# Optimization experiments

Measured on AMD Instinct MI355X. Metric: run time of the kernel, lower is better.

Reference implementation:

```python
import jax, jax.numpy as jnp
import numpy as np

C = 4096
C8 = C // 8  # 512, must equal h*w
B, H, W = 32, 16, 32


def setup_inputs() -> dict:
    key = jax.random.key(0)
    ks = jax.random.split(key, 8)
    s = 0.02
    return {
        "x": jax.random.normal(ks[0], (B, C, H, W), dtype=jnp.float32),
        "Wq": jax.random.normal(ks[1], (C8, C), dtype=jnp.float32) * s,
        "bq": jax.random.normal(ks[2], (C8,), dtype=jnp.float32) * s,
        "Wk": jax.random.normal(ks[3], (C8, C), dtype=jnp.float32) * s,
        "bk": jax.random.normal(ks[4], (C8,), dtype=jnp.float32) * s,
        "Wv": jax.random.normal(ks[5], (C, C), dtype=jnp.float32) * s,
        "bv": jax.random.normal(ks[6], (C,), dtype=jnp.float32) * s,
        "gamma": jax.random.normal(ks[7], (1,), dtype=jnp.float32),
    }


def reference(x, Wq, bq, Wk, bk, Wv, bv, gamma):
    b, c, h, w = x.shape
    xf = x.reshape(b, c, h * w)               # (b, c, hw)
    # 1x1 conv == per-position linear over channels
    q = jnp.einsum("oc,bcl->bol", Wq, xf) + bq[None, :, None]   # (b, c8, hw)
    k = jnp.einsum("oc,bcl->bol", Wk, xf) + bk[None, :, None]   # (b, c8, hw)
    v = jnp.einsum("oc,bcl->bol", Wv, xf) + bv[None, :, None]   # (b, c, hw)
    # energy = bmm(Q, K^T): (b, c8, c8); no sqrt(d) scaling (faithful)
    energy = jnp.einsum("bol,bpl->bop", q, k)
    attn = jax.nn.softmax(energy, axis=-1)
    # out = bmm(V, attn^T): out[b,c,p] = sum_k V[b,c,k] * attn[b,p,k]
    out = jnp.einsum("bck,bpk->bcp", v, attn)  # requires hw == c8
    out = out.reshape(b, c, h, w)
    return gamma * out + x
```

## Files before the change

### kernel.cpp

```cpp
#include <hip/hip_runtime.h>


typedef _Float16 f16;
typedef _Float16 h8 __attribute__((ext_vector_type(8)));
typedef _Float16 h4 __attribute__((ext_vector_type(4)));
typedef float fx4 __attribute__((ext_vector_type(4)));

#define CC  4096
#define C8  512
#define HWD 512
#define NB  32


__device__ __forceinline__ h8 ldfragC(const char* s, int row, int cb) {
  const int b = ((row << 7) | cb) ^ ((row & 7) << 4);
  return *reinterpret_cast<const h8*>(s + b);
}

#define AS1C(p) ((const __attribute__((address_space(1))) unsigned int*)(p))
#define AS3(p)  ((__attribute__((address_space(3))) unsigned int*)(p))

#define STAGE(bufsel) { \
  char* la_ = smem + ((bufsel) << 16); \
  char* lb_ = la_ + 32768; \
  _Pragma("unroll") for (int q = 0; q < 4; ++q) { \
    __builtin_amdgcn_global_load_lds(AS1C(pA[q]), AS3(la_ + (q << 13) + w1024), 16, 0, 0); \
    __builtin_amdgcn_global_load_lds(AS1C(pB[q]), AS3(lb_ + (q << 13) + w1024), 16, 0, 0); \
    pA[q] += 128; pB[q] += 128; } }

#define LOADA(hm, kh) { \
  _Pragma("unroll") for (int f = 0; f < 4; ++f) \
    a[f] = ldfragC(At, wr * 128 + (hm) * 64 + f * 16 + frow, (kh) * 64 + kq); }

#define LOADB(kh) { \
  _Pragma("unroll") for (int g = 0; g < 4; ++g) \
    b[g] = ldfragC(Bt, wc * 64 + g * 16 + frow, (kh) * 64 + kq); }

#define PHASE(hm) { \
  asm volatile("s_barrier" ::: "memory"); \
  asm volatile("s_waitcnt lgkmcnt(0)" ::: "memory"); \
  __builtin_amdgcn_sched_barrier(0); \
  __builtin_amdgcn_s_setprio(1); \
  _Pragma("unroll") for (int f = 0; f < 4; ++f) \
  _Pragma("unroll") for (int g = 0; g < 4; ++g) \
    acc[(hm) * 4 + f][g] = __builtin_amdgcn_mfma_f32_16x16x32_f16( \
        a[f], b[g], acc[(hm) * 4 + f][g], 0, 0, 0); \
  __builtin_amdgcn_s_setprio(0); \
  asm volatile("s_barrier" ::: "memory"); }

template<int EPI>
__global__ __launch_bounds__(512, 2) void gemm256(
    const f16* __restrict__ Ah, const f16* __restrict__ Bh,
    int lda, int ldb, long sAb, long sBb, long sCb, int ldc, int K,
    const float* __restrict__ bias, float* __restrict__ Cf, f16* __restrict__ Ch,
    const float* __restrict__ resid, const float* __restrict__ gam)
{
  extern __shared__ __align__(16) char smem[];
  const int F  = blockIdx.x;
  const int Vv = ((F & 7) << 7) | (F >> 3);
  const int bz = Vv >> 5;
  const int m0 = (Vv & 15) << 8;
  const int n0 = ((Vv >> 4) & 1) << 8;

  const int T = threadIdx.x;
  const int lane = T & 63;
  const int w = T >> 6;
  const int wr = w >> 2, wc = w & 3;
  const int frow = lane & 15;
  const int kq = (lane >> 4) << 4;
  const int w1024 = w << 10;

  const int rr = T >> 3;
  const int corig = ((T & 7) << 4) ^ ((rr & 7) << 4);
  const char* pA[4];
  const char* pB[4];
#pragma unroll
  for (int q = 0; q < 4; ++q) {
    pA[q] = (const char*)(Ah + bz * sAb + (long)(m0 + q * 64 + rr) * lda) + corig;
    pB[q] = (const char*)(Bh + bz * sBb + (long)(n0 + q * 64 + rr) * ldb) + corig;
  }

  fx4 acc[8][4] = {};
  const int nt = K >> 6;

  STAGE(0)
  for (int t = 0; t < nt; ++t) {
    const int cur = t & 1;
    if (t + 1 < nt) {
      STAGE(cur ^ 1)
      asm volatile("s_waitcnt vmcnt(8)" ::: "memory");
    } else {
      asm volatile("s_waitcnt vmcnt(0)" ::: "memory");
    }
    asm volatile("s_barrier" ::: "memory");
    const char* At = smem + (cur << 16);
    const char* Bt = At + 32768;
    h8 a[4], b[4];
    LOADA(0, 0) LOADB(0)
    PHASE(0)
    LOADA(1, 0)
    PHASE(1)
    LOADA(0, 1) LOADB(1)
    PHASE(0)
    LOADA(1, 1)
    PHASE(1)
  }

  const int cm = (lane >> 4) << 2;
  const int cn = lane & 15;
  const float g0 = (EPI == 3) ? gam[0] : 0.f;
#pragma unroll
  for (int fm = 0; fm < 8; ++fm) {
    const int gr0 = m0 + wr * 128 + fm * 16 + cm;
#pragma unroll
    for (int fn = 0; fn < 4; ++fn) {
      const int gc = n0 + wc * 64 + fn * 16 + cn;
#pragma unroll
      for (int j = 0; j < 4; ++j) {
        const long ci = bz * sCb + (long)(gr0 + j) * ldc + gc;
        if constexpr (EPI == 1) Ch[ci] = (f16)(acc[fm][fn][j] + bias[gr0 + j]);
        else                    Cf[ci] = g0 * acc[fm][fn][j] + resid[ci];
      }
    }
  }
}

__device__ __forceinline__ void stage_tile(const f16* __restrict__ g, f16* __restrict__ s, int ld) {
  const int t = threadIdx.x;
#pragma unroll
  for (int i = 0; i < 4; ++i) {
    const int id = t + i * 256;
    const int r = id >> 3, j = id & 7;
    const uint4 v = *reinterpret_cast<const uint4*>(g + (long)r * ld + (j << 3));
    char* p = reinterpret_cast<char*>(s);
    const int b = ((r << 7) + (j << 4)) ^ ((r & 7) << 4);
    *reinterpret_cast<uint4*>(p + b) = v;
  }
}

__device__ __forceinline__ h8 ldfrag(const f16* s, int row, int kb) {
  const int b = ((row << 7) + kb) ^ ((row & 7) << 4);
  return *reinterpret_cast<const h8*>(reinterpret_cast<const char*>(s) + b);
}

template<int EPI>
__global__ __launch_bounds__(256) void gemm_tri(
    const f16* __restrict__ Ah, const f16* __restrict__ Al,
    const f16* __restrict__ Bh, const f16* __restrict__ Bl,
    int K, int lda, int ldb, long sAb, long sBb, long sCb, int ldc,
    const float* __restrict__ bias,
    float* __restrict__ Cf, f16* __restrict__ Ch, f16* __restrict__ Cl)
{
  constexpr int TILE = 128 * 64;
  __shared__ __align__(16) f16 smem[4 * TILE];
  f16* sAh = smem;
  f16* sBh = smem + TILE;
  f16* sAl = smem + 2 * TILE;
  f16* sBl = smem + 3 * TILE;

  const int bz = blockIdx.z;
  const int m0 = blockIdx.y * 128, n0 = blockIdx.x * 128;
  const f16* gA = Ah + (long)bz * sAb + (long)m0 * lda;
  const f16* gB = Bh + (long)bz * sBb + (long)n0 * ldb;

  const int lane = threadIdx.x & 63;
  const int wid  = threadIdx.x >> 6;
  const int wr = wid >> 1, wc = wid & 1;
  const int frow = lane & 15;
  const int kq = (lane >> 4) << 4;

  fx4 acc[4][4] = {};

  for (int k0 = 0; k0 < K; k0 += 64) {
    stage_tile(gA + k0, sAh, lda);
    stage_tile(gB + k0, sBh, ldb);
    stage_tile(Al + (long)bz * sAb + (long)m0 * lda + k0, sAl, lda);
    stage_tile(Bl + (long)bz * sBb + (long)n0 * ldb + k0, sBl, ldb);
    __syncthreads();
#pragma unroll
    for (int ks = 0; ks < 2; ++ks) {
      const int kb = ks * 64 + kq;
      h8 aH[4], bH[4], aL[4], bL[4];
#pragma unroll
      for (int f = 0; f < 4; ++f) {
        aH[f] = ldfrag(sAh, wr * 64 + f * 16 + frow, kb);
        bH[f] = ldfrag(sBh, wc * 64 + f * 16 + frow, kb);
        aL[f] = ldfrag(sAl, wr * 64 + f * 16 + frow, kb);
        bL[f] = ldfrag(sBl, wc * 64 + f * 16 + frow, kb);
      }
#pragma unroll
      for (int fm = 0; fm < 4; ++fm)
#pragma unroll
        for (int fn = 0; fn < 4; ++fn) {
          acc[fm][fn] = __builtin_amdgcn_mfma_f32_16x16x32_f16(aH[fm], bH[fn], acc[fm][fn], 0, 0, 0);
          acc[fm][fn] = __builtin_amdgcn_mfma_f32_16x16x32_f16(aH[fm], bL[fn], acc[fm][fn], 0, 0, 0);
          acc[fm][fn] = __builtin_amdgcn_mfma_f32_16x16x32_f16(aL[fm], bH[fn], acc[fm][fn], 0, 0, 0);
        }
    }
    __syncthreads();
  }

  const int cm = (lane >> 4) * 4;
  const int cn = lane & 15;
#pragma unroll
  for (int fm = 0; fm < 4; ++fm) {
    const int gr0 = m0 + wr * 64 + fm * 16 + cm;
#pragma unroll
    for (int fn = 0; fn < 4; ++fn) {
      const int gc = n0 + wc * 64 + fn * 16 + cn;
#pragma unroll
      for (int j = 0; j < 4; ++j) {
        const int gr = gr0 + j;
        const long ci = (long)bz * sCb + (long)gr * ldc + gc;
        float v = acc[fm][fn][j];
        if constexpr (EPI == 0) {
          v += bias[gr];
          const f16 h = (f16)v;
          Ch[ci] = h;
          Cl[ci] = (f16)(v - (float)h);
        } else {
          Cf[ci] = v;
        }
      }
    }
  }
}

__global__ void transpose_split_k(const float* __restrict__ x, f16* __restrict__ xh, f16* __restrict__ xl) {
  __shared__ float t[32][33];
  const int l0 = blockIdx.x * 32, c0 = blockIdx.y * 32;
  const long bi = (long)blockIdx.z * CC * HWD;
  const long bo = (long)blockIdx.z * HWD * CC;
  const int tx = threadIdx.x, ty = threadIdx.y;
#pragma unroll
  for (int i = 0; i < 32; i += 8)
    t[ty + i][tx] = x[bi + (long)(c0 + ty + i) * HWD + l0 + tx];
  __syncthreads();
#pragma unroll
  for (int i = 0; i < 32; i += 8) {
    const float v = t[tx][ty + i];
    const f16 h = (f16)v;
    const long o = bo + (long)(l0 + ty + i) * CC + c0 + tx;
    xh[o] = h;
    xl[o] = (f16)(v - (float)h);
  }
}

template<bool HASLO>
__global__ void split_k(const float* __restrict__ in, f16* __restrict__ hi, f16* __restrict__ lo, long n) {
  const long i = ((long)blockIdx.x * blockDim.x + threadIdx.x) * 4;
  if (i >= n) return;
  const float4 v = *reinterpret_cast<const float4*>(in + i);
  const float vv[4] = {v.x, v.y, v.z, v.w};
  h4 h, l;
#pragma unroll
  for (int j = 0; j < 4; ++j) {
    const f16 hh = (f16)vv[j];
    h[j] = hh;
    l[j] = (f16)(vv[j] - (float)hh);
  }
  *reinterpret_cast<h4*>(hi + i) = h;
  if constexpr (HASLO) *reinterpret_cast<h4*>(lo + i) = l;
}

__global__ __launch_bounds__(256) void softmax_k(const float* __restrict__ E, f16* __restrict__ attn) {
  const int lane = threadIdx.x & 63;
  const int wid  = threadIdx.x >> 6;
  const long row = (long)blockIdx.x * 4 + wid;
  const float* e = E + row * 512;
  const float4 a = *reinterpret_cast<const float4*>(e + lane * 8);
  const float4 b = *reinterpret_cast<const float4*>(e + lane * 8 + 4);
  float vv[8] = {a.x, a.y, a.z, a.w, b.x, b.y, b.z, b.w};
  float m = vv[0];
#pragma unroll
  for (int i = 1; i < 8; ++i) m = fmaxf(m, vv[i]);
#pragma unroll
  for (int s = 32; s > 0; s >>= 1) m = fmaxf(m, __shfl_xor(m, s));
  float sum = 0.f;
  float ex[8];
#pragma unroll
  for (int i = 0; i < 8; ++i) { ex[i] = __expf(vv[i] - m); sum += ex[i]; }
#pragma unroll
  for (int s = 32; s > 0; s >>= 1) sum += __shfl_xor(sum, s);
  const float inv = 1.f / sum;
  h8 o;
#pragma unroll
  for (int i = 0; i < 8; ++i) o[i] = (f16)(ex[i] * inv);
  *reinterpret_cast<h8*>(attn + row * 512 + lane * 8) = o;
}

extern "C" void kernel_launch(void* const* d_in, const int* in_sizes, int n_in,
                              void* d_out, int out_size, void* d_ws, size_t ws_size,
                              hipStream_t stream) {
  const float* x  = (const float*)d_in[0];
  const float* Wq = (const float*)d_in[1];
  const float* bq = (const float*)d_in[2];
  const float* Wk = (const float*)d_in[3];
  const float* bk = (const float*)d_in[4];
  const float* Wv = (const float*)d_in[5];
  const float* bv = (const float*)d_in[6];
  const float* gm = (const float*)d_in[7];
  float* out = (float*)d_out;

  const size_t szXT = (size_t)NB * HWD * CC;
  const size_t szQK = (size_t)NB * C8 * HWD;
  const size_t szW  = (size_t)C8 * CC;
  const size_t szWv = (size_t)CC * CC;
  const size_t needBytes = (2 * szXT + 4 * szQK + 4 * szW + szWv) * sizeof(f16);
  if (ws_size < needBytes) return;

  f16* xT_h = (f16*)d_ws;
  f16* xT_l = xT_h + szXT;
  f16* v16  = xT_l;
  f16* q_h  = xT_h + 2 * szXT;
  f16* q_l  = q_h + szQK;
  f16* k_h  = q_l + szQK;
  f16* k_l  = k_h + szQK;
  f16* wq_h = k_l + szQK;
  f16* wq_l = wq_h + szW;
  f16* wk_h = wq_l + szW;
  f16* wk_l = wk_h + szW;
  f16* attn = wq_h;
  f16* wv_h = wk_l + szW;
  float* E  = (float*)wv_h;

  split_k<true ><<<dim3((C8 * CC) / 1024), 256, 0, stream>>>(Wq, wq_h, wq_l, (long)C8 * CC);
  split_k<true ><<<dim3((C8 * CC) / 1024), 256, 0, stream>>>(Wk, wk_h, wk_l, (long)C8 * CC);
  split_k<false><<<dim3((CC * CC) / 1024), 256, 0, stream>>>(Wv, wv_h, nullptr, (long)CC * CC);
  transpose_split_k<<<dim3(HWD / 32, CC / 32, NB), dim3(32, 8), 0, stream>>>(x, xT_h, xT_l);
  gemm_tri<0><<<dim3(4, 4, NB), 256, 0, stream>>>(wq_h, wq_l, xT_h, xT_l, CC, CC, CC,
      0L, (long)HWD * CC, (long)C8 * HWD, HWD, bq, nullptr, q_h, q_l);
  gemm_tri<0><<<dim3(4, 4, NB), 256, 0, stream>>>(wk_h, wk_l, xT_h, xT_l, CC, CC, CC,
      0L, (long)HWD * CC, (long)C8 * HWD, HWD, bk, nullptr, k_h, k_l);
  gemm256<1><<<dim3(1024), 512, 131072, stream>>>(wv_h, xT_h, CC, CC,
      0L, (long)HWD * CC, (long)CC * HWD, HWD, CC, bv, nullptr, v16, nullptr, nullptr);
  gemm_tri<2><<<dim3(4, 4, NB), 256, 0, stream>>>(q_h, q_l, k_h, k_l, HWD, HWD, HWD,
      (long)C8 * HWD, (long)C8 * HWD, (long)C8 * C8, C8, nullptr, E, nullptr, nullptr);
  softmax_k<<<dim3(NB * C8 / 4), 256, 0, stream>>>(E, attn);
  gemm256<3><<<dim3(1024), 512, 131072, stream>>>(v16, attn, HWD, HWD,
      (long)CC * HWD, (long)C8 * HWD, (long)CC * HWD, HWD, C8, nullptr, out, nullptr, x, gm);
}
```

Baseline: 1.384 ms.

## Interleave next-tile global-to-LDS prefetch across MMA phases in GEMM main loop

Restructures the K loop so the global_load_lds prefetch of the next tile is split into pieces issued between the LDS fragment reads and MFMA phases, rather than all at once at the top of each iteration. Fragment registers are double-buffered (a0/a1, b0/b1), and the loop is unrolled by two with a fixed buffer index per half. The aim is to spread memory traffic across compute and overlap it better. The trade-off is a full vmcnt(0) wait at each tile start and more barriers, which may expose load latency. The unroll assumes an even number of K tiles.

```diff
diff --git a/kernel.cpp b/kernel.cpp
--- a/kernel.cpp
+++ b/kernel.cpp
@@ -20,7 +20,7 @@
 #define AS1C(p) ((const __attribute__((address_space(1))) unsigned int*)(p))
 #define AS3(p)  ((__attribute__((address_space(3))) unsigned int*)(p))
 
-#define STAGE(bufsel) { \
+#define STAGE_ALL(bufsel) { \
   char* la_ = smem + ((bufsel) << 16); \
   char* lb_ = la_ + 32768; \
   _Pragma("unroll") for (int q = 0; q < 4; ++q) { \
@@ -28,25 +28,63 @@
     __builtin_amdgcn_global_load_lds(AS1C(pB[q]), AS3(lb_ + (q << 13) + w1024), 16, 0, 0); \
     pA[q] += 128; pB[q] += 128; } }
 
-#define LOADA(hm, kh) { \
+#define STAGE2(bufsel, q) { \
+  char* la_ = smem + ((bufsel) << 16); \
+  char* lb_ = la_ + 32768; \
+  __builtin_amdgcn_global_load_lds(AS1C(pA[q]), AS3(la_ + ((q) << 13) + w1024), 16, 0, 0); \
+  __builtin_amdgcn_global_load_lds(AS1C(pB[q]), AS3(lb_ + ((q) << 13) + w1024), 16, 0, 0); \
+  pA[q] += 128; pB[q] += 128; }
+
+#define DSREADS_A(dst, hm, kh) \
   _Pragma("unroll") for (int f = 0; f < 4; ++f) \
-    a[f] = ldfragC(At, wr * 128 + (hm) * 64 + f * 16 + frow, (kh) * 64 + kq); }
-
-#define LOADB(kh) { \
+    dst[f] = ldfragC(At, wr * 128 + (hm) * 64 + f * 16 + frow, (kh) * 64 + kq);
+
+#define DSREADS_B(dst, kh) \
   _Pragma("unroll") for (int g = 0; g < 4; ++g) \
-    b[g] = ldfragC(Bt, wc * 64 + g * 16 + frow, (kh) * 64 + kq); }
-
-#define PHASE(hm) { \
-  asm volatile("s_barrier" ::: "memory"); \
-  asm volatile("s_waitcnt lgkmcnt(0)" ::: "memory"); \
-  __builtin_amdgcn_sched_barrier(0); \
+    dst[g] = ldfragC(Bt, wc * 64 + g * 16 + frow, (kh) * 64 + kq);
+
+#define MMA16(hm, av, bv) \
   __builtin_amdgcn_s_setprio(1); \
   _Pragma("unroll") for (int f = 0; f < 4; ++f) \
   _Pragma("unroll") for (int g = 0; g < 4; ++g) \
     acc[(hm) * 4 + f][g] = __builtin_amdgcn_mfma_f32_16x16x32_f16( \
-        a[f], b[g], acc[(hm) * 4 + f][g], 0, 0, 0); \
-  __builtin_amdgcn_s_setprio(0); \
-  asm volatile("s_barrier" ::: "memory"); }
+        av[f], bv[g], acc[(hm) * 4 + f][g], 0, 0, 0); \
+  __builtin_amdgcn_s_setprio(0);
+
+#define KTILE(cur, DOSTAGE) { \
+  const bool dost_ = (DOSTAGE); \
+  const char* At = smem + ((cur) << 16); \
+  const char* Bt = At + 32768; \
+  h8 a0[4], a1[4], b0[4], b1[4]; \
+  asm volatile("s_waitcnt vmcnt(0)" ::: "memory"); \
+  __builtin_amdgcn_s_barrier(); \
+   \
+  DSREADS_A(a0, 0, 0) DSREADS_B(b0, 0) \
+  if (dost_) { STAGE2((cur) ^ 1, 0) STAGE2((cur) ^ 1, 1) } \
+  __builtin_amdgcn_s_barrier(); \
+  asm volatile("s_waitcnt lgkmcnt(0)"); \
+  MMA16(0, a0, b0) \
+  __builtin_amdgcn_s_barrier(); \
+   \
+  DSREADS_A(a1, 1, 0) \
+  if (dost_) { STAGE2((cur) ^ 1, 2) STAGE2((cur) ^ 1, 3) } \
+  __builtin_amdgcn_s_barrier(); \
+  asm volatile("s_waitcnt lgkmcnt(0)"); \
+  MMA16(1, a1, b0) \
+  __builtin_amdgcn_s_barrier(); \
+   \
+  DSREADS_A(a0, 0, 1) DSREADS_B(b1, 1) \
+  __builtin_amdgcn_s_barrier(); \
+  asm volatile("s_waitcnt lgkmcnt(0)"); \
+  MMA16(0, a0, b1) \
+  __builtin_amdgcn_s_barrier(); \
+   \
+  DSREADS_A(a1, 1, 1) \
+  __builtin_amdgcn_s_barrier(); \
+  asm volatile("s_waitcnt lgkmcnt(0)"); \
+  MMA16(1, a1, b1) \
+  __builtin_amdgcn_s_barrier(); \
+}
 
 template<int EPI>
 __global__ __launch_bounds__(512, 2) void gemm256(
@@ -83,27 +121,10 @@
   fx4 acc[8][4] = {};
   const int nt = K >> 6;
 
-  STAGE(0)
-  for (int t = 0; t < nt; ++t) {
-    const int cur = t & 1;
-    if (t + 1 < nt) {
-      STAGE(cur ^ 1)
-      asm volatile("s_waitcnt vmcnt(8)" ::: "memory");
-    } else {
-      asm volatile("s_waitcnt vmcnt(0)" ::: "memory");
-    }
-    asm volatile("s_barrier" ::: "memory");
-    const char* At = smem + (cur << 16);
-    const char* Bt = At + 32768;
-    h8 a[4], b[4];
-    LOADA(0, 0) LOADB(0)
-    PHASE(0)
-    LOADA(1, 0)
-    PHASE(1)
-    LOADA(0, 1) LOADB(1)
-    PHASE(0)
-    LOADA(1, 1)
-    PHASE(1)
+  STAGE_ALL(0)
+  for (int t = 0; t < nt; t += 2) {
+    KTILE(0, t + 1 < nt)
+    KTILE(1, t + 2 < nt)
   }
 
   const int cm = (lane >> 4) << 2;
```

Measured after the change: 1.299 ms. 6.2% less time.
